# Performance work log

Measured on AMD Instinct MI355X. Metric: run time of the kernel, lower is better.

## Reference

```python
import jax, jax.numpy as jnp
import numpy as np

N_NODES = 20000
N_EDGES = 640000
HIDDEN = 128


def setup_inputs() -> dict:
    key = jax.random.key(0)
    k1, k2, k3, k4 = jax.random.split(key, 4)
    scale = 1.0 / np.sqrt(HIDDEN)
    features = jax.random.normal(k1, (N_NODES, HIDDEN), dtype=jnp.float32)
    edge_index = jax.random.randint(k2, (2, N_EDGES), 0, N_NODES, dtype=jnp.int64)
    W_l = jax.random.normal(k3, (HIDDEN, HIDDEN), dtype=jnp.float32) * scale
    b_l = jnp.zeros((HIDDEN,), dtype=jnp.float32)
    W_r = jax.random.normal(k4, (HIDDEN, HIDDEN), dtype=jnp.float32) * scale
    return {"features": features, "edge_index": edge_index, "W_l": W_l, "b_l": b_l, "W_r": W_r}


def reference(features, edge_index, W_l, b_l, W_r):
    # PyG SAGEConv with mean aggregation:
    #   out_i = lin_l(mean_{j : (j->i) in E} x_j) + lin_r(x_i)
    # edge_index[0] = source nodes, edge_index[1] = target nodes.
    n = features.shape[0]
    src = edge_index[0]
    dst = edge_index[1]
    msg = features[src]  # [E, d] gather
    summed = jax.ops.segment_sum(msg, dst, num_segments=n)  # [N, d] scatter-add
    cnt = jax.ops.segment_sum(jnp.ones(src.shape[0], dtype=features.dtype), dst, num_segments=n)
    agg = summed / jnp.maximum(cnt, 1.0)[:, None]  # mean; isolated nodes -> 0
    return agg @ W_l.T + b_l + features @ W_r.T
```

## Files before the change

### kernel.cpp

```cpp
#include <hip/hip_runtime.h>

#define N_NODES 20000
#define N_EDGES 640000
#define HIDDEN  128
#define CAP     96
#define DEG_PAD 16

typedef unsigned short bf16_t;
typedef __attribute__((ext_vector_type(8))) short short8;
typedef __attribute__((ext_vector_type(4))) float floatx4;

__device__ __forceinline__ bf16_t f2bf(float f) {
    union { float f; unsigned int i; } v; v.f = f;
    unsigned int x = v.i + 0x7FFFu + ((v.i >> 16) & 1u);
    return (bf16_t)(x >> 16);
}
__device__ __forceinline__ float bflo(unsigned u) {
    union { unsigned i; float f; } v; v.i = u << 16; return v.f;
}
__device__ __forceinline__ float bfhi(unsigned u) {
    union { unsigned i; float f; } v; v.i = u & 0xFFFF0000u; return v.f;
}
__device__ __forceinline__ unsigned pack2(float x, float y) {
    return (unsigned)f2bf(x) | ((unsigned)f2bf(y) << 16);
}

__global__ void prep_kernel(const float* __restrict__ feat,
                            const float* __restrict__ Wl,
                            const float* __restrict__ Wr,
                            bf16_t* __restrict__ feat_bf,
                            bf16_t* __restrict__ Bp) {
    int t = blockIdx.x * 256 + threadIdx.x;
    if (t < (N_NODES * HIDDEN) / 4) {
        float4 v = ((const float4*)feat)[t];
        ushort4 o = { f2bf(v.x), f2bf(v.y), f2bf(v.z), f2bf(v.w) };
        ((ushort4*)feat_bf)[t] = o;
    }
    if (t < 2 * HIDDEN * HIDDEN) {
        int j    = t & 7;
        int lane = (t >> 3) & 63;
        int nt   = (t >> 9) & 7;
        int kt   = t >> 12;
        int n = nt * 16 + (lane & 15);
        int k = kt * 32 + (lane >> 4) * 8 + j;
        float v = (k < HIDDEN) ? Wl[n * HIDDEN + k] : Wr[n * HIDDEN + (k - HIDDEN)];
        Bp[t] = f2bf(v);
    }
}

__global__ void bucket_fill_kernel(const int* __restrict__ eidx,
                                   int* __restrict__ deg,
                                   int* __restrict__ bucket) {
    int e = blockIdx.x * 256 + threadIdx.x;
    if (e >= N_EDGES) return;
    int src = eidx[e];
    int dst = eidx[N_EDGES + e];
    int pos = atomicAdd(&deg[dst * DEG_PAD], 1);
    if (pos < CAP) bucket[dst * CAP + pos] = src;
}

__global__ __launch_bounds__(256) void gather_kernel(
        const bf16_t* __restrict__ feat_bf,
        const int* __restrict__ deg,
        const int* __restrict__ bucket,
        bf16_t* __restrict__ agg_bf) {
    int wid  = (blockIdx.x * 256 + threadIdx.x) >> 6;
    int lane = threadIdx.x & 63;
    if (wid >= N_NODES) return;
    int d_true = deg[wid * DEG_PAD];
    int d = min(d_true, CAP);
    const int* row = bucket + wid * CAP;
    const unsigned* f = (const unsigned*)feat_bf;
    float ax0=0,ay0=0, ax1=0,ay1=0, ax2=0,ay2=0, ax3=0,ay3=0;
    int i = 0;
    for (; i + 4 <= d; i += 4) {
        int4 s = *(const int4*)(row + i);
        unsigned u0 = f[s.x * 64 + lane];
        unsigned u1 = f[s.y * 64 + lane];
        unsigned u2 = f[s.z * 64 + lane];
        unsigned u3 = f[s.w * 64 + lane];
        ax0 += bflo(u0); ay0 += bfhi(u0);
        ax1 += bflo(u1); ay1 += bfhi(u1);
        ax2 += bflo(u2); ay2 += bfhi(u2);
        ax3 += bflo(u3); ay3 += bfhi(u3);
    }
    for (; i < d; ++i) {
        unsigned u = f[row[i] * 64 + lane];
        ax0 += bflo(u); ay0 += bfhi(u);
    }
    float inv = 1.0f / fmaxf((float)d_true, 1.0f);
    float x = (ax0 + ax1 + ax2 + ax3) * inv;
    float y = (ay0 + ay1 + ay2 + ay3) * inv;
    ((unsigned*)agg_bf)[wid * 64 + lane] = pack2(x, y);
}

__global__ __launch_bounds__(256) void gemm_mfma_kernel(
        const bf16_t* __restrict__ agg_bf,
        const bf16_t* __restrict__ feat_bf,
        const bf16_t* __restrict__ Bp,
        const float* __restrict__ bl,
        float* __restrict__ out) {
    int wid = blockIdx.x * 4 + (threadIdx.x >> 6);
    if (wid >= N_NODES / 16) return;
    int lane = threadIdx.x & 63;
    int m    = lane & 15;
    int quad = lane >> 4;
    int row0 = wid * 16;

    floatx4 acc[8];
    floatx4 z = {0.f, 0.f, 0.f, 0.f};
#pragma unroll
    for (int nt = 0; nt < 8; ++nt) acc[nt] = z;

    const short8* bp = (const short8*)Bp;
#pragma unroll
    for (int kt = 0; kt < 8; ++kt) {
        const bf16_t* asrc = (kt < 4) ? agg_bf : feat_bf;
        int koff = (kt & 3) * 32 + quad * 8;
        short8 afrag = *(const short8*)(asrc + (size_t)(row0 + m) * HIDDEN + koff);
#pragma unroll
        for (int nt = 0; nt < 8; ++nt) {
            short8 bfrag = bp[(kt * 8 + nt) * 64 + lane];
            acc[nt] = __builtin_amdgcn_mfma_f32_16x16x32_bf16(afrag, bfrag, acc[nt], 0, 0, 0);
        }
    }

    int col = lane & 15;
#pragma unroll
    for (int nt = 0; nt < 8; ++nt) {
        float b = bl[nt * 16 + col];
#pragma unroll
        for (int r = 0; r < 4; ++r) {
            int row = row0 + quad * 4 + r;
            out[(size_t)row * HIDDEN + nt * 16 + col] = acc[nt][r] + b;
        }
    }
}

extern "C" void kernel_launch(void* const* d_in, const int* in_sizes, int n_in,
                              void* d_out, int out_size, void* d_ws, size_t ws_size,
                              hipStream_t stream) {
    const float* feat = (const float*)d_in[0];
    const int*   eidx = (const int*)d_in[1];
    const float* Wl   = (const float*)d_in[2];
    const float* bl   = (const float*)d_in[3];
    const float* Wr   = (const float*)d_in[4];
    float* out = (float*)d_out;

    int*    deg     = (int*)d_ws;
    int*    bucket  = deg + N_NODES * DEG_PAD;
    bf16_t* Bp      = (bf16_t*)(bucket + N_NODES * CAP);
    bf16_t* feat_bf = Bp + 2 * HIDDEN * HIDDEN;
    bf16_t* agg_bf  = feat_bf + (size_t)N_NODES * HIDDEN;

    hipMemsetAsync(deg, 0, (size_t)N_NODES * DEG_PAD * sizeof(int), stream);

    prep_kernel<<<2500, 256, 0, stream>>>(feat, Wl, Wr, feat_bf, Bp);
    bucket_fill_kernel<<<(N_EDGES + 255) / 256, 256, 0, stream>>>(eidx, deg, bucket);
    gather_kernel<<<(N_NODES * 64 + 255) / 256, 256, 0, stream>>>(feat_bf, deg, bucket, agg_bf);
    gemm_mfma_kernel<<<(N_NODES / 16 + 3) / 4, 256, 0, stream>>>(agg_bf, feat_bf, Bp, bl, out);
}
```

Before: 140.1 us.

## Transform-then-aggregate: GEMM before gather, co-launch GEMM with bucket fill

Reorders the SAGE computation so features are first multiplied by both weight matrices. The W_l product is stored in bf16 and the W_r product plus bias in fp32, and the mean aggregation then runs over the transformed rows with the residual added in the final gather. The GEMM and the edge bucket-fill are merged into one launch, and the degree memset is folded into the prep kernel, which removes launches and lets the two phases overlap. In exchange, aggregation now sums bf16-rounded transformed values, which shifts numerical error, and an extra fp32 Z buffer is written and read.

Result: no change. 142.1 us (+1.5%).

```diff
diff --git a/kernel.cpp b/kernel.cpp
--- a/kernel.cpp
+++ b/kernel.cpp
@@ -5,6 +5,8 @@
 #define HIDDEN  128
 #define CAP     96
 #define DEG_PAD 16
+#define GEMM_BLOCKS 313
+#define FILL_BLOCKS 2500
 
 typedef unsigned short bf16_t;
 typedef __attribute__((ext_vector_type(8))) short short8;
@@ -21,120 +23,130 @@
 __device__ __forceinline__ float bfhi(unsigned u) {
     union { unsigned i; float f; } v; v.i = u & 0xFFFF0000u; return v.f;
 }
-__device__ __forceinline__ unsigned pack2(float x, float y) {
-    return (unsigned)f2bf(x) | ((unsigned)f2bf(y) << 16);
-}
 
 __global__ void prep_kernel(const float* __restrict__ feat,
                             const float* __restrict__ Wl,
                             const float* __restrict__ Wr,
                             bf16_t* __restrict__ feat_bf,
-                            bf16_t* __restrict__ Bp) {
+                            bf16_t* __restrict__ Bp,
+                            int* __restrict__ deg) {
     int t = blockIdx.x * 256 + threadIdx.x;
-    if (t < (N_NODES * HIDDEN) / 4) {
-        float4 v = ((const float4*)feat)[t];
-        ushort4 o = { f2bf(v.x), f2bf(v.y), f2bf(v.z), f2bf(v.w) };
-        ((ushort4*)feat_bf)[t] = o;
+    float4 v = ((const float4*)feat)[t];
+    ushort4 o = { f2bf(v.x), f2bf(v.y), f2bf(v.z), f2bf(v.w) };
+    ((ushort4*)feat_bf)[t] = o;
+    if (t < (N_NODES * DEG_PAD) / 4) {
+        int4 zz = {0, 0, 0, 0};
+        ((int4*)deg)[t] = zz;
     }
     if (t < 2 * HIDDEN * HIDDEN) {
         int j    = t & 7;
         int lane = (t >> 3) & 63;
-        int nt   = (t >> 9) & 7;
-        int kt   = t >> 12;
+        int nt   = (t >> 9) & 15;
+        int kt   = t >> 13;
         int n = nt * 16 + (lane & 15);
         int k = kt * 32 + (lane >> 4) * 8 + j;
-        float v = (k < HIDDEN) ? Wl[n * HIDDEN + k] : Wr[n * HIDDEN + (k - HIDDEN)];
-        Bp[t] = f2bf(v);
+        float w = (n < HIDDEN) ? Wl[n * HIDDEN + k] : Wr[(n - HIDDEN) * HIDDEN + k];
+        Bp[t] = f2bf(w);
     }
 }
 
-__global__ void bucket_fill_kernel(const int* __restrict__ eidx,
-                                   int* __restrict__ deg,
-                                   int* __restrict__ bucket) {
-    int e = blockIdx.x * 256 + threadIdx.x;
-    if (e >= N_EDGES) return;
-    int src = eidx[e];
-    int dst = eidx[N_EDGES + e];
-    int pos = atomicAdd(&deg[dst * DEG_PAD], 1);
-    if (pos < CAP) bucket[dst * CAP + pos] = src;
+__global__ __launch_bounds__(256) void gemm_fill_kernel(
+        const bf16_t* __restrict__ feat_bf,
+        const bf16_t* __restrict__ Bp,
+        const float* __restrict__ bl,
+        const int* __restrict__ eidx,
+        bf16_t* __restrict__ Y,
+        float* __restrict__ Z,
+        int* __restrict__ deg,
+        int* __restrict__ bucket) {
+    if (blockIdx.x < GEMM_BLOCKS) {
+        int wid = blockIdx.x * 4 + (threadIdx.x >> 6);
+        if (wid >= N_NODES / 16) return;
+        int lane = threadIdx.x & 63;
+        int m    = lane & 15;
+        int quad = lane >> 4;
+        int row0 = wid * 16;
+
+        floatx4 acc[16];
+        floatx4 zf = {0.f, 0.f, 0.f, 0.f};
+#pragma unroll
+        for (int nt = 0; nt < 16; ++nt) acc[nt] = zf;
+
+        const short8* bp = (const short8*)Bp;
+#pragma unroll
+        for (int kt = 0; kt < 4; ++kt) {
+            short8 afrag = *(const short8*)(feat_bf + (size_t)(row0 + m) * HIDDEN
+                                            + kt * 32 + quad * 8);
+#pragma unroll
+            for (int nt = 0; nt < 16; ++nt) {
+                short8 bfrag = bp[(kt * 16 + nt) * 64 + lane];
+                acc[nt] = __builtin_amdgcn_mfma_f32_16x16x32_bf16(afrag, bfrag, acc[nt], 0, 0, 0);
+            }
+        }
+        int col = lane & 15;
+#pragma unroll
+        for (int nt = 0; nt < 8; ++nt) {
+#pragma unroll
+            for (int r = 0; r < 4; ++r) {
+                int row = row0 + quad * 4 + r;
+                Y[(size_t)row * HIDDEN + nt * 16 + col] = f2bf(acc[nt][r]);
+            }
+        }
+#pragma unroll
+        for (int nt = 8; nt < 16; ++nt) {
+            float b = bl[(nt - 8) * 16 + col];
+#pragma unroll
+            for (int r = 0; r < 4; ++r) {
+                int row = row0 + quad * 4 + r;
+                Z[(size_t)row * HIDDEN + (nt - 8) * 16 + col] = acc[nt][r] + b;
+            }
+        }
+    } else {
+        int e = (blockIdx.x - GEMM_BLOCKS) * 256 + threadIdx.x;
+        if (e >= N_EDGES) return;
+        int src = eidx[e];
+        int dst = eidx[N_EDGES + e];
+        int pos = atomicAdd(&deg[dst * DEG_PAD], 1);
+        if (pos < CAP) bucket[dst * CAP + pos] = src;
+    }
 }
 
-__global__ __launch_bounds__(256) void gather_kernel(
-        const bf16_t* __restrict__ feat_bf,
+__global__ __launch_bounds__(256) void gather_final_kernel(
+        const bf16_t* __restrict__ Y,
+        const float* __restrict__ Z,
         const int* __restrict__ deg,
         const int* __restrict__ bucket,
-        bf16_t* __restrict__ agg_bf) {
+        float* __restrict__ out) {
     int wid  = (blockIdx.x * 256 + threadIdx.x) >> 6;
     int lane = threadIdx.x & 63;
     if (wid >= N_NODES) return;
     int d_true = deg[wid * DEG_PAD];
     int d = min(d_true, CAP);
     const int* row = bucket + wid * CAP;
-    const unsigned* f = (const unsigned*)feat_bf;
+    const unsigned* y = (const unsigned*)Y;
     float ax0=0,ay0=0, ax1=0,ay1=0, ax2=0,ay2=0, ax3=0,ay3=0;
     int i = 0;
     for (; i + 4 <= d; i += 4) {
         int4 s = *(const int4*)(row + i);
-        unsigned u0 = f[s.x * 64 + lane];
-        unsigned u1 = f[s.y * 64 + lane];
-        unsigned u2 = f[s.z * 64 + lane];
-        unsigned u3 = f[s.w * 64 + lane];
+        unsigned u0 = y[s.x * 64 + lane];
+        unsigned u1 = y[s.y * 64 + lane];
+        unsigned u2 = y[s.z * 64 + lane];
+        unsigned u3 = y[s.w * 64 + lane];
         ax0 += bflo(u0); ay0 += bfhi(u0);
         ax1 += bflo(u1); ay1 += bfhi(u1);
         ax2 += bflo(u2); ay2 += bfhi(u2);
         ax3 += bflo(u3); ay3 += bfhi(u3);
     }
     for (; i < d; ++i) {
-        unsigned u = f[row[i] * 64 + lane];
+        unsigned u = y[row[i] * 64 + lane];
         ax0 += bflo(u); ay0 += bfhi(u);
     }
     float inv = 1.0f / fmaxf((float)d_true, 1.0f);
-    float x = (ax0 + ax1 + ax2 + ax3) * inv;
-    float y = (ay0 + ay1 + ay2 + ay3) * inv;
-    ((unsigned*)agg_bf)[wid * 64 + lane] = pack2(x, y);
-}
-
-__global__ __launch_bounds__(256) void gemm_mfma_kernel(
-        const bf16_t* __restrict__ agg_bf,
-        const bf16_t* __restrict__ feat_bf,
-        const bf16_t* __restrict__ Bp,
-        const float* __restrict__ bl,
-        float* __restrict__ out) {
-    int wid = blockIdx.x * 4 + (threadIdx.x >> 6);
-    if (wid >= N_NODES / 16) return;
-    int lane = threadIdx.x & 63;
-    int m    = lane & 15;
-    int quad = lane >> 4;
-    int row0 = wid * 16;
-
-    floatx4 acc[8];
-    floatx4 z = {0.f, 0.f, 0.f, 0.f};
-#pragma unroll
-    for (int nt = 0; nt < 8; ++nt) acc[nt] = z;
-
-    const short8* bp = (const short8*)Bp;
-#pragma unroll
-    for (int kt = 0; kt < 8; ++kt) {
-        const bf16_t* asrc = (kt < 4) ? agg_bf : feat_bf;
-        int koff = (kt & 3) * 32 + quad * 8;
-        short8 afrag = *(const short8*)(asrc + (size_t)(row0 + m) * HIDDEN + koff);
-#pragma unroll
-        for (int nt = 0; nt < 8; ++nt) {
-            short8 bfrag = bp[(kt * 8 + nt) * 64 + lane];
-            acc[nt] = __builtin_amdgcn_mfma_f32_16x16x32_bf16(afrag, bfrag, acc[nt], 0, 0, 0);
-        }
-    }
-
-    int col = lane & 15;
-#pragma unroll
-    for (int nt = 0; nt < 8; ++nt) {
-        float b = bl[nt * 16 + col];
-#pragma unroll
-        for (int r = 0; r < 4; ++r) {
-            int row = row0 + quad * 4 + r;
-            out[(size_t)row * HIDDEN + nt * 16 + col] = acc[nt][r] + b;
-        }
-    }
+    float2 z = ((const float2*)Z)[wid * 64 + lane];
+    float2 r;
+    r.x = (ax0 + ax1 + ax2 + ax3) * inv + z.x;
+    r.y = (ay0 + ay1 + ay2 + ay3) * inv + z.y;
+    ((float2*)out)[wid * 64 + lane] = r;
 }
 
 extern "C" void kernel_launch(void* const* d_in, const int* in_sizes, int n_in,
@@ -151,12 +163,12 @@
     int*    bucket  = deg + N_NODES * DEG_PAD;
     bf16_t* Bp      = (bf16_t*)(bucket + N_NODES * CAP);
     bf16_t* feat_bf = Bp + 2 * HIDDEN * HIDDEN;
-    bf16_t* agg_bf  = feat_bf + (size_t)N_NODES * HIDDEN;
+    bf16_t* Y       = feat_bf + (size_t)N_NODES * HIDDEN;
+    float*  Z       = (float*)(Y + (size_t)N_NODES * HIDDEN);
 
-    hipMemsetAsync(deg, 0, (size_t)N_NODES * DEG_PAD * sizeof(int), stream);
-
-    prep_kernel<<<2500, 256, 0, stream>>>(feat, Wl, Wr, feat_bf, Bp);
-    bucket_fill_kernel<<<(N_EDGES + 255) / 256, 256, 0, stream>>>(eidx, deg, bucket);
-    gather_kernel<<<(N_NODES * 64 + 255) / 256, 256, 0, stream>>>(feat_bf, deg, bucket, agg_bf);
-    gemm_mfma_kernel<<<(N_NODES / 16 + 3) / 4, 256, 0, stream>>>(agg_bf, feat_bf, Bp, bl, out);
+    prep_kernel<<<2500, 256, 0, stream>>>(feat, Wl, Wr, feat_bf, Bp, deg);
+    gemm_fill_kernel<<<GEMM_BLOCKS + FILL_BLOCKS, 256, 0, stream>>>(
+        feat_bf, Bp, bl, eidx, Y, Z, deg, bucket);
+    gather_final_kernel<<<(N_NODES * 64 + 255) / 256, 256, 0, stream>>>(
+        Y, Z, deg, bucket, out);
 }
```
